# Performance work log

Hardware: AMD Instinct MI355X
Metric: run time of the kernel (lower is better)

Reference implementation:

```python
import jax, jax.numpy as jnp
import numpy as np

# Dimensions matching init_kwargs
O = 4096   # out_features
I = 4096   # in_features
R = 32     # svd_rank
G = 64     # n_groups
GS = I // G  # group_size = 64
NBITS = 4
NUM_BYTES = O * I * NBITS // 8


def setup_inputs() -> dict:
    key = jax.random.key(0)
    ks = jax.random.split(key, 7)
    return {
        "x": jax.random.normal(ks[0], (1, 4096, I), dtype=jnp.float32),
        # bit-packed int4 weights, two nibbles per byte (stored as int32 holding 0..255)
        "w_packed": jax.random.randint(ks[1], (NUM_BYTES,), 0, 256, dtype=jnp.int32),
        "svd_up": jax.random.normal(ks[2], (O, R), dtype=jnp.float32) * 0.02,
        "svd_down": jax.random.normal(ks[3], (R, I), dtype=jnp.float32) * 0.02,
        "scale": jax.random.uniform(ks[4], (O, G, 1), dtype=jnp.float32, minval=0.001, maxval=0.02),
        "zero_point": jax.random.uniform(ks[5], (O, G, 1), dtype=jnp.float32, minval=0.0, maxval=15.0),
        "bias": jax.random.normal(ks[6], (O,), dtype=jnp.float32) * 0.01,
    }


def _dequantize(w_packed, svd_up, svd_down, scale, zero_point):
    # Unpack two 4-bit values per byte (low nibble first).
    low = w_packed & 0xF
    high = (w_packed >> 4) & 0xF
    w_q = jnp.stack([low, high], axis=-1).reshape(O, G, GS).astype(jnp.float32)
    # Per-group affine dequant: (q - zero) * scale, then SVD low-rank correction.
    W = ((w_q - zero_point) * scale).reshape(O, I)
    return W + svd_up @ svd_down  # [O, I]


def reference(x, w_packed, svd_up, svd_down, scale, zero_point, bias):
    # forward_int8 path (tokens > 16, int8_matmul=True)
    W_f = _dequantize(w_packed, svd_up, svd_down, scale, zero_point).T  # [I, O]
    xm = x.reshape(-1, I)  # [N, I]
    # Dynamic per-row activation quant
    scale_x = jnp.max(jnp.abs(xm), axis=1, keepdims=True) / 127.0  # [N, 1]
    x_q = jnp.clip(jnp.round(xm / scale_x), -128, 127).astype(jnp.int8)
    # Dynamic per-column weight quant
    scale_w = jnp.max(jnp.abs(W_f), axis=0, keepdims=True) / 127.0  # [1, O]
    W_q = jnp.clip(jnp.round(W_f / scale_w), -128, 127).astype(jnp.int8)
    # int8 GEMM with int32 accumulation, then dequant scales + bias
    acc = jnp.matmul(x_q.astype(jnp.int32), W_q.astype(jnp.int32))  # [N, O] int32
    out = acc.astype(jnp.float32) * scale_x * scale_w + bias
    return out.reshape(*x.shape[:-1], O)
```

## Files before the change

### kernel.cpp

```cpp
#include <hip/hip_runtime.h>
#include <cstdint>
#include <cstddef>

#define I_DIM 4096
#define O_DIM 4096
#define RNK 32
#define NGRP 64
#define N_TOK 4096

typedef int v4i __attribute__((ext_vector_type(4)));

__device__ __forceinline__ int clamp_i8(float v) {
    int q = (int)rintf(v);
    q = q < -128 ? -128 : q;
    q = q > 127 ? 127 : q;
    return q;
}

#define BO 4

__global__ __launch_bounds__(256, 4) void quant_w_kernel(
    const int* __restrict__ w_packed, const float* __restrict__ svd_up,
    const float* __restrict__ svd_down, const float* __restrict__ scale,
    const float* __restrict__ zp, char* __restrict__ w_q,
    float* __restrict__ scale_w)
{
    __shared__ float s_sc[BO][NGRP];
    __shared__ float s_zp[BO][NGRP];
    __shared__ float s_red[BO][4];
    __shared__ float s_sw[BO];

    const int tid = threadIdx.x;
    const int o0 = blockIdx.x * BO;

    for (int t = tid; t < BO * NGRP; t += 256) {
        s_sc[t >> 6][t & 63] = scale[(size_t)(o0 + (t >> 6)) * NGRP + (t & 63)];
        s_zp[t >> 6][t & 63] = zp[(size_t)(o0 + (t >> 6)) * NGRP + (t & 63)];
    }
    __syncthreads();

    float W[4][BO][4];
    float vmax[BO];
#pragma unroll
    for (int ro = 0; ro < BO; ro++) vmax[ro] = 0.0f;

#pragma unroll
    for (int jq = 0; jq < 4; jq++) {
        const int q = tid + 256 * jq;
        const int i = 4 * q;
        const int g = q >> 4;

#pragma unroll
        for (int ro = 0; ro < BO; ro++) {
            const int2 b2 = *(const int2*)&w_packed[(size_t)(o0 + ro) * (I_DIM / 2) + 2 * q];
            const float sc = s_sc[ro][g], z = s_zp[ro][g];
            W[jq][ro][0] = ((float)(b2.x & 0xF) - z) * sc;
            W[jq][ro][1] = ((float)((b2.x >> 4) & 0xF) - z) * sc;
            W[jq][ro][2] = ((float)(b2.y & 0xF) - z) * sc;
            W[jq][ro][3] = ((float)((b2.y >> 4) & 0xF) - z) * sc;
        }

#pragma unroll 4
        for (int r = 0; r < RNK; r++) {
            const float4 d = *(const float4*)&svd_down[(size_t)r * I_DIM + i];
#pragma unroll
            for (int ro = 0; ro < BO; ro++) {
                const float u = svd_up[(size_t)(o0 + ro) * RNK + r];
                W[jq][ro][0] += u * d.x;
                W[jq][ro][1] += u * d.y;
                W[jq][ro][2] += u * d.z;
                W[jq][ro][3] += u * d.w;
            }
        }

#pragma unroll
        for (int ro = 0; ro < BO; ro++) {
            vmax[ro] = fmaxf(vmax[ro],
                fmaxf(fmaxf(fabsf(W[jq][ro][0]), fabsf(W[jq][ro][1])),
                      fmaxf(fabsf(W[jq][ro][2]), fabsf(W[jq][ro][3]))));
        }
    }

    const int lane = tid & 63, wv = tid >> 6;
#pragma unroll
    for (int ro = 0; ro < BO; ro++) {
        float m = vmax[ro];
        for (int off = 32; off > 0; off >>= 1)
            m = fmaxf(m, __shfl_down(m, off, 64));
        if (lane == 0) s_red[ro][wv] = m;
    }
    __syncthreads();
    if (tid < BO) {
        const float m = fmaxf(fmaxf(s_red[tid][0], s_red[tid][1]),
                              fmaxf(s_red[tid][2], s_red[tid][3]));
        const float sw = m / 127.0f;
        scale_w[o0 + tid] = sw;
        s_sw[tid] = sw;
    }
    __syncthreads();

    float inv[BO];
#pragma unroll
    for (int ro = 0; ro < BO; ro++) inv[ro] = 1.0f / s_sw[ro];

#pragma unroll
    for (int jq = 0; jq < 4; jq++) {
        const int q = tid + 256 * jq;
#pragma unroll
        for (int ro = 0; ro < BO; ro++) {
            const int q0 = clamp_i8(W[jq][ro][0] * inv[ro]);
            const int q1 = clamp_i8(W[jq][ro][1] * inv[ro]);
            const int q2 = clamp_i8(W[jq][ro][2] * inv[ro]);
            const int q3 = clamp_i8(W[jq][ro][3] * inv[ro]);
            ((int*)w_q)[(size_t)(o0 + ro) * (I_DIM / 4) + q] =
                (q0 & 0xFF) | ((q1 & 0xFF) << 8) | ((q2 & 0xFF) << 16) | ((q3 & 0xFF) << 24);
        }
    }
}

__global__ __launch_bounds__(256) void quant_x_kernel(
    const float* __restrict__ x, char* __restrict__ x_q,
    float* __restrict__ scale_x)
{
    const int n = blockIdx.x;
    const int tid = threadIdx.x;
    const float4* xr = (const float4*)(x + (size_t)n * I_DIM);
    float4 v[4];
    float m = 0.0f;
#pragma unroll
    for (int j = 0; j < 4; j++) {
        v[j] = xr[tid + 256 * j];
        m = fmaxf(m, fmaxf(fmaxf(fabsf(v[j].x), fabsf(v[j].y)),
                           fmaxf(fabsf(v[j].z), fabsf(v[j].w))));
    }
    __shared__ float s_red[4];
    __shared__ float s_sx;
    for (int off = 32; off > 0; off >>= 1)
        m = fmaxf(m, __shfl_down(m, off, 64));
    if ((tid & 63) == 0) s_red[tid >> 6] = m;
    __syncthreads();
    if (tid == 0) {
        const float mm = fmaxf(fmaxf(s_red[0], s_red[1]),
                               fmaxf(s_red[2], s_red[3]));
        const float sx = mm / 127.0f;
        scale_x[n] = sx;
        s_sx = sx;
    }
    __syncthreads();
    const float sx = s_sx;
    int* outw = (int*)(x_q + (size_t)n * I_DIM);
#pragma unroll
    for (int j = 0; j < 4; j++) {
        const int q0 = clamp_i8(v[j].x / sx);
        const int q1 = clamp_i8(v[j].y / sx);
        const int q2 = clamp_i8(v[j].z / sx);
        const int q3 = clamp_i8(v[j].w / sx);
        outw[tid + 256 * j] =
            (q0 & 0xFF) | ((q1 & 0xFF) << 8) | ((q2 & 0xFF) << 16) | ((q3 & 0xFF) << 24);
    }
}

#define BM 128
#define BN 128
#define BK 128

__global__ __launch_bounds__(256) void gemm_i8_kernel(
    const char* __restrict__ x_q, const char* __restrict__ w_q,
    const float* __restrict__ scale_x, const float* __restrict__ scale_w,
    const float* __restrict__ bias, float* __restrict__ out)
{
    __shared__ v4i As4[BM * BK / 16];
    __shared__ v4i Bs4[BN * BK / 16];
    char* As = (char*)As4;
    char* Bs = (char*)Bs4;

    const int tid = threadIdx.x;
    const int bm0 = blockIdx.x * BM;
    const int bn0 = blockIdx.y * BN;
    const int lane = tid & 63, wv = tid >> 6;
    const int wm = wv & 1, wn = wv >> 1;
    const int quad = lane >> 4, l15 = lane & 15;

    v4i acc[4][4];
#pragma unroll
    for (int mt = 0; mt < 4; mt++)
#pragma unroll
        for (int nt = 0; nt < 4; nt++)
            acc[mt][nt] = (v4i){0, 0, 0, 0};

    for (int kk = 0; kk < I_DIM / BK; kk++) {
        const int k0 = kk * BK;
#pragma unroll
        for (int j = 0; j < 4; j++) {
            const int c = tid + 256 * j;
            const int row = c >> 3;
            const int kc = (c & 7) ^ (row & 7);
            const char* ga = x_q + (size_t)(bm0 + row) * I_DIM + k0 + kc * 16;
            __builtin_amdgcn_global_load_lds(
                (const __attribute__((address_space(1))) unsigned int*)ga,
                (__attribute__((address_space(3))) unsigned int*)(As + c * 16),
                16, 0, 0);
            const char* gb = w_q + (size_t)(bn0 + row) * I_DIM + k0 + kc * 16;
            __builtin_amdgcn_global_load_lds(
                (const __attribute__((address_space(1))) unsigned int*)gb,
                (__attribute__((address_space(3))) unsigned int*)(Bs + c * 16),
                16, 0, 0);
        }
        __syncthreads();
#pragma unroll
        for (int s = 0; s < 2; s++) {
            v4i af[4], bf[4];
#pragma unroll
            for (int mt = 0; mt < 4; mt++) {
                const int row = wm * 64 + mt * 16 + l15;
                const int kc = (s * 4 + quad) ^ (l15 & 7);
                af[mt] = *(const v4i*)(As + row * BK + kc * 16);
            }
#pragma unroll
            for (int nt = 0; nt < 4; nt++) {
                const int row = wn * 64 + nt * 16 + l15;
                const int kc = (s * 4 + quad) ^ (l15 & 7);
                bf[nt] = *(const v4i*)(Bs + row * BK + kc * 16);
            }
#pragma unroll
            for (int mt = 0; mt < 4; mt++)
#pragma unroll
                for (int nt = 0; nt < 4; nt++)
                    acc[mt][nt] = __builtin_amdgcn_mfma_i32_16x16x64_i8(
                        af[mt], bf[nt], acc[mt][nt], 0, 0, 0);
        }
        __syncthreads();
    }

#pragma unroll
    for (int mt = 0; mt < 4; mt++) {
        const int n0 = bm0 + wm * 64 + mt * 16 + quad * 4;
        float sx[4];
#pragma unroll
        for (int r = 0; r < 4; r++) sx[r] = scale_x[n0 + r];
#pragma unroll
        for (int nt = 0; nt < 4; nt++) {
            const int oc = bn0 + wn * 64 + nt * 16 + l15;
            const float sw = scale_w[oc];
            const float bs = bias[oc];
#pragma unroll
            for (int r = 0; r < 4; r++) {
                out[(size_t)(n0 + r) * O_DIM + oc] =
                    (float)acc[mt][nt][r] * sx[r] * sw + bs;
            }
        }
    }
}

extern "C" void kernel_launch(void* const* d_in, const int* in_sizes, int n_in,
                              void* d_out, int out_size, void* d_ws, size_t ws_size,
                              hipStream_t stream) {
    const float* x        = (const float*)d_in[0];
    const int*   w_packed = (const int*)d_in[1];
    const float* svd_up   = (const float*)d_in[2];
    const float* svd_down = (const float*)d_in[3];
    const float* scale    = (const float*)d_in[4];
    const float* zp       = (const float*)d_in[5];
    const float* bias     = (const float*)d_in[6];
    float* out = (float*)d_out;

    char* ws = (char*)d_ws;
    char*  w_q     = ws;
    char*  x_q     = ws + ((size_t)16 << 20);
    float* scale_w = (float*)(ws + ((size_t)32 << 20));
    float* scale_x = (float*)(ws + ((size_t)32 << 20) + 16384);

    quant_w_kernel<<<O_DIM / BO, 256, 0, stream>>>(w_packed, svd_up, svd_down,
                                                   scale, zp, w_q, scale_w);
    quant_x_kernel<<<N_TOK, 256, 0, stream>>>(x, x_q, scale_x);
    gemm_i8_kernel<<<dim3(N_TOK / BM, O_DIM / BN), 256, 0, stream>>>(
        x_q, w_q, scale_x, scale_w, bias, out);
}
```

Baseline: 254.7 us.

## Switch int8 GEMM to 32x32x32 MFMA and restructure SVD correction loop

The int8 GEMM inner loop now uses 32x32x32 i8 MFMA tiles (2x2 per wave) in place of 16x16x64 tiles (4x4 per wave), with new fragment indexing and a new epilogue mapping for the 16-register accumulator layout. The aim is fewer LDS fragment loads per MFMA and higher throughput per instruction. The weight-quant kernel stages svd_up in shared memory and moves the rank loop outside the column loop so each svd_down row is loaded once per rank. Its occupancy hint in launch_bounds is also dropped. The larger MFMA shape changes the store pattern of the epilogue and may lengthen instruction latency.

```diff
diff --git a/kernel.cpp b/kernel.cpp
--- a/kernel.cpp
+++ b/kernel.cpp
@@ -8,7 +8,8 @@
 #define NGRP 64
 #define N_TOK 4096
 
-typedef int v4i __attribute__((ext_vector_type(4)));
+typedef int v4i  __attribute__((ext_vector_type(4)));
+typedef int v16i __attribute__((ext_vector_type(16)));
 
 __device__ __forceinline__ int clamp_i8(float v) {
     int q = (int)rintf(v);
@@ -19,7 +20,7 @@
 
 #define BO 4
 
-__global__ __launch_bounds__(256, 4) void quant_w_kernel(
+__global__ __launch_bounds__(256) void quant_w_kernel(
     const int* __restrict__ w_packed, const float* __restrict__ svd_up,
     const float* __restrict__ svd_down, const float* __restrict__ scale,
     const float* __restrict__ zp, char* __restrict__ w_q,
@@ -27,12 +28,17 @@
 {
     __shared__ float s_sc[BO][NGRP];
     __shared__ float s_zp[BO][NGRP];
+    __shared__ float s_up[RNK][BO];
     __shared__ float s_red[BO][4];
     __shared__ float s_sw[BO];
 
     const int tid = threadIdx.x;
     const int o0 = blockIdx.x * BO;
 
+    if (tid < RNK * BO) {
+        const int r = tid >> 2, ro = tid & 3;
+        s_up[r][ro] = svd_up[(size_t)(o0 + ro) * RNK + r];
+    }
     for (int t = tid; t < BO * NGRP; t += 256) {
         s_sc[t >> 6][t & 63] = scale[(size_t)(o0 + (t >> 6)) * NGRP + (t & 63)];
         s_zp[t >> 6][t & 63] = zp[(size_t)(o0 + (t >> 6)) * NGRP + (t & 63)];
@@ -40,16 +46,11 @@
     __syncthreads();
 
     float W[4][BO][4];
-    float vmax[BO];
-#pragma unroll
-    for (int ro = 0; ro < BO; ro++) vmax[ro] = 0.0f;
 
 #pragma unroll
     for (int jq = 0; jq < 4; jq++) {
         const int q = tid + 256 * jq;
-        const int i = 4 * q;
         const int g = q >> 4;
-
 #pragma unroll
         for (int ro = 0; ro < BO; ro++) {
             const int2 b2 = *(const int2*)&w_packed[(size_t)(o0 + ro) * (I_DIM / 2) + 2 * q];
@@ -59,27 +60,39 @@
             W[jq][ro][2] = ((float)(b2.y & 0xF) - z) * sc;
             W[jq][ro][3] = ((float)((b2.y >> 4) & 0xF) - z) * sc;
         }
-
-#pragma unroll 4
-        for (int r = 0; r < RNK; r++) {
-            const float4 d = *(const float4*)&svd_down[(size_t)r * I_DIM + i];
+    }
+
+#pragma unroll 2
+    for (int r = 0; r < RNK; r++) {
+        const float4* dr = (const float4*)(svd_down + (size_t)r * I_DIM);
+        float u[BO];
+#pragma unroll
+        for (int ro = 0; ro < BO; ro++) u[ro] = s_up[r][ro];
+        float4 d[4];
+#pragma unroll
+        for (int jq = 0; jq < 4; jq++) d[jq] = dr[tid + 256 * jq];
+#pragma unroll
+        for (int jq = 0; jq < 4; jq++) {
 #pragma unroll
             for (int ro = 0; ro < BO; ro++) {
-                const float u = svd_up[(size_t)(o0 + ro) * RNK + r];
-                W[jq][ro][0] += u * d.x;
-                W[jq][ro][1] += u * d.y;
-                W[jq][ro][2] += u * d.z;
-                W[jq][ro][3] += u * d.w;
-            }
-        }
-
-#pragma unroll
-        for (int ro = 0; ro < BO; ro++) {
+                W[jq][ro][0] += u[ro] * d[jq].x;
+                W[jq][ro][1] += u[ro] * d[jq].y;
+                W[jq][ro][2] += u[ro] * d[jq].z;
+                W[jq][ro][3] += u[ro] * d[jq].w;
+            }
+        }
+    }
+
+    float vmax[BO];
+#pragma unroll
+    for (int ro = 0; ro < BO; ro++) vmax[ro] = 0.0f;
+#pragma unroll
+    for (int jq = 0; jq < 4; jq++)
+#pragma unroll
+        for (int ro = 0; ro < BO; ro++)
             vmax[ro] = fmaxf(vmax[ro],
                 fmaxf(fmaxf(fabsf(W[jq][ro][0]), fabsf(W[jq][ro][1])),
                       fmaxf(fabsf(W[jq][ro][2]), fabsf(W[jq][ro][3]))));
-        }
-    }
 
     const int lane = tid & 63, wv = tid >> 6;
 #pragma unroll
@@ -179,14 +192,14 @@
     const int bn0 = blockIdx.y * BN;
     const int lane = tid & 63, wv = tid >> 6;
     const int wm = wv & 1, wn = wv >> 1;
-    const int quad = lane >> 4, l15 = lane & 15;
-
-    v4i acc[4][4];
-#pragma unroll
-    for (int mt = 0; mt < 4; mt++)
-#pragma unroll
-        for (int nt = 0; nt < 4; nt++)
-            acc[mt][nt] = (v4i){0, 0, 0, 0};
+    const int l31 = lane & 31, h = lane >> 5;
+
+    v16i acc[2][2];
+#pragma unroll
+    for (int mt = 0; mt < 2; mt++)
+#pragma unroll
+        for (int nt = 0; nt < 2; nt++)
+            acc[mt][nt] = (v16i)(0);
 
     for (int kk = 0; kk < I_DIM / BK; kk++) {
         const int k0 = kk * BK;
@@ -208,45 +221,47 @@
         }
         __syncthreads();
 #pragma unroll
-        for (int s = 0; s < 2; s++) {
-            v4i af[4], bf[4];
-#pragma unroll
-            for (int mt = 0; mt < 4; mt++) {
-                const int row = wm * 64 + mt * 16 + l15;
-                const int kc = (s * 4 + quad) ^ (l15 & 7);
+        for (int s = 0; s < 4; s++) {
+            v4i af[2], bf[2];
+#pragma unroll
+            for (int mt = 0; mt < 2; mt++) {
+                const int row = wm * 64 + mt * 32 + l31;
+                const int kc = (s * 2 + h) ^ (row & 7);
                 af[mt] = *(const v4i*)(As + row * BK + kc * 16);
             }
 #pragma unroll
-            for (int nt = 0; nt < 4; nt++) {
-                const int row = wn * 64 + nt * 16 + l15;
-                const int kc = (s * 4 + quad) ^ (l15 & 7);
+            for (int nt = 0; nt < 2; nt++) {
+                const int row = wn * 64 + nt * 32 + l31;
+                const int kc = (s * 2 + h) ^ (row & 7);
                 bf[nt] = *(const v4i*)(Bs + row * BK + kc * 16);
             }
 #pragma unroll
-            for (int mt = 0; mt < 4; mt++)
-#pragma unroll
-                for (int nt = 0; nt < 4; nt++)
-                    acc[mt][nt] = __builtin_amdgcn_mfma_i32_16x16x64_i8(
+            for (int mt = 0; mt < 2; mt++)
+#pragma unroll
+                for (int nt = 0; nt < 2; nt++)
+                    acc[mt][nt] = __builtin_amdgcn_mfma_i32_32x32x32_i8(
                         af[mt], bf[nt], acc[mt][nt], 0, 0, 0);
         }
         __syncthreads();
     }
 
 #pragma unroll
-    for (int mt = 0; mt < 4; mt++) {
-        const int n0 = bm0 + wm * 64 + mt * 16 + quad * 4;
-        float sx[4];
-#pragma unroll
-        for (int r = 0; r < 4; r++) sx[r] = scale_x[n0 + r];
-#pragma unroll
-        for (int nt = 0; nt < 4; nt++) {
-            const int oc = bn0 + wn * 64 + nt * 16 + l15;
+    for (int mt = 0; mt < 2; mt++) {
+        const int rbase = bm0 + wm * 64 + mt * 32 + 4 * h;
+        float sx[16];
+#pragma unroll
+        for (int reg = 0; reg < 16; reg++)
+            sx[reg] = scale_x[rbase + (reg & 3) + 8 * (reg >> 2)];
+#pragma unroll
+        for (int nt = 0; nt < 2; nt++) {
+            const int oc = bn0 + wn * 64 + nt * 32 + l31;
             const float sw = scale_w[oc];
             const float bs = bias[oc];
 #pragma unroll
-            for (int r = 0; r < 4; r++) {
-                out[(size_t)(n0 + r) * O_DIM + oc] =
-                    (float)acc[mt][nt][r] * sx[r] * sw + bs;
+            for (int reg = 0; reg < 16; reg++) {
+                const int rr = rbase + (reg & 3) + 8 * (reg >> 2);
+                out[(size_t)rr * O_DIM + oc] =
+                    (float)acc[mt][nt][reg] * sx[reg] * sw + bs;
             }
         }
     }
```

Result: slower. 263.3 us (+3.4%).
